# Performance work log

Measured on AMD Instinct MI355X. Metric: run time of the kernel, lower is better.

## Reference

```python
import jax, jax.numpy as jnp
import numpy as np

B = 2048          # batch (vmapped samples)
STEPS = 64        # hardcoded scan length in module
H = 64            # hidden_size
W = 128           # width_size
NZ = 32           # noise_size (control_size)
INZ = 32          # initial_noise_size
D = 8             # data_size


def lipswish(x):
    return 0.909 * jax.nn.silu(x)


def _mlp3(x, W0, b0, W1, b1, W2, b2, act, final_act):
    # eqx.nn.MLP with depth=2: in->width, width->width, width->out
    h = act(x @ W0.T + b0)
    h = act(h @ W1.T + b1)
    return final_act(h @ W2.T + b2)


def setup_inputs() -> dict:
    key = jax.random.key(0)
    ks = jax.random.split(key, 32)

    def lin(k, out_d, in_d):
        lim = 1.0 / np.sqrt(in_d)
        kw, kb = jax.random.split(k)
        Wm = jax.random.uniform(kw, (out_d, in_d), minval=-lim, maxval=lim, dtype=jnp.float32)
        bv = jax.random.uniform(kb, (out_d,), minval=-lim, maxval=lim, dtype=jnp.float32)
        return Wm, bv

    Wi0, bi0 = lin(ks[0], W, INZ)
    Wi1, bi1 = lin(ks[1], W, W)
    Wi2, bi2 = lin(ks[2], H, W)

    Wv0, bv0 = lin(ks[3], W, H + 1)
    Wv1, bv1 = lin(ks[4], W, W)
    Wv2, bv2 = lin(ks[5], H, W)
    scale_v = jax.random.uniform(ks[6], (H,), minval=0.9, maxval=1.1, dtype=jnp.float32)

    Wc0, bc0 = lin(ks[7], W, H + 1)
    Wc1, bc1 = lin(ks[8], W, W)
    Wc2, bc2 = lin(ks[9], H * NZ, W)
    scale_c = jax.random.uniform(ks[10], (H, NZ), minval=0.9, maxval=1.1, dtype=jnp.float32)

    Wr, br = lin(ks[11], D, H)

    ts = jnp.arange(STEPS + 1, dtype=jnp.float32)
    init_noise = jax.random.normal(ks[12], (B, INZ), dtype=jnp.float32)
    bm = jax.random.normal(ks[13], (B, STEPS, NZ), dtype=jnp.float32)

    return dict(ts=ts, init_noise=init_noise, bm=bm,
                Wi0=Wi0, bi0=bi0, Wi1=Wi1, bi1=bi1, Wi2=Wi2, bi2=bi2,
                scale_v=scale_v, Wv0=Wv0, bv0=bv0, Wv1=Wv1, bv1=bv1, Wv2=Wv2, bv2=bv2,
                scale_c=scale_c, Wc0=Wc0, bc0=bc0, Wc1=Wc1, bc1=bc1, Wc2=Wc2, bc2=bc2,
                Wr=Wr, br=br)


def reference(ts, init_noise, bm,
              Wi0, bi0, Wi1, bi1, Wi2, bi2,
              scale_v, Wv0, bv0, Wv1, bv1, Wv2, bv2,
              scale_c, Wc0, bc0, Wc1, bc1, Wc2, bc2,
              Wr, br):
    t0 = ts[0]
    dt = jnp.float32(1.0)  # dt0 hardcoded in module
    sqrt_dt = jnp.sqrt(dt)

    # initial MLP (relu hidden, identity final): noise -> y0 [B,H]
    y0 = _mlp3(init_noise, Wi0, bi0, Wi1, bi1, Wi2, bi2, jax.nn.relu, lambda x: x)

    bm_t = jnp.transpose(bm, (1, 0, 2))  # [STEPS, B, NZ]
    idx = jnp.arange(STEPS, dtype=jnp.float32)

    def step(y, xs):
        i, bm_i = xs
        t = t0 + i * dt
        tcol = jnp.broadcast_to(jnp.reshape(t, (1, 1)), (y.shape[0], 1))
        inp = jnp.concatenate([tcol, y], axis=1)  # [B, H+1]
        # drift vector field
        drift = scale_v * _mlp3(inp, Wv0, bv0, Wv1, bv1, Wv2, bv2, lipswish, jnp.tanh)
        # controlled vector field: [B, H, NZ]
        diff = scale_c * _mlp3(inp, Wc0, bc0, Wc1, bc1, Wc2, bc2, lipswish, jnp.tanh).reshape(-1, H, NZ)
        y1 = y + drift * dt + jnp.einsum('bhn,bn->bh', diff, bm_i * sqrt_dt)
        return y1, y1

    _, ys = jax.lax.scan(step, y0, (idx, bm_t), length=STEPS, unroll=8)  # ys [STEPS,B,H]
    out = jnp.einsum('tbh,dh->tbd', ys, Wr) + br  # readout per step
    return jnp.transpose(out, (1, 0, 2))  # [B, STEPS, D]
```

## Files before the change

kernel.cpp:

```cpp
#include <hip/hip_runtime.h>
#include <stdint.h>
#include <stddef.h>


typedef __attribute__((ext_vector_type(8))) short bf16x8;
typedef __attribute__((ext_vector_type(4))) float f32x4;
typedef __attribute__((ext_vector_type(4))) int   i32x4;

#define BB 16
#define NWG 256

#define WS_WI0 0
#define WS_WI1 8192
#define WS_WI2 40960
#define WS_WV0 57344
#define WS_WV1 73728
#define WS_WV2 106496
#define WS_WC0 122880
#define WS_WC1 139264
#define WS_WC2 172032
#define WS_TV0 696320
#define WS_TC0 696832
#define WS_XCHG 700416
#define WS_FLAG 2273280

#define LD_WV0 0
#define LD_WV1 16384
#define LD_WC0 49152
#define LD_WC1 65536
#define LD_YBF 98304
#define LD_H1V 100352
#define LD_H1C 104448
#define LD_H2V 108544
#define LD_H2C 112640
#define LD_Y   116736
#define LD_DB  121088
#define LD_BM  125440
#define LD_BSC 127552
#define LD_BEV 135744
#define LD_BEC 136256
#define LD_BV1 136768
#define LD_BC1 137280
#define LD_BV2 137792
#define LD_SV  138048
#define LD_WR  138304
#define LD_BR  140480
#define LD_WV2 140512
#define LD_DFL 148704
#define LDS_TOTAL 148712

__device__ __forceinline__ short f2bf(float f) {
  uint32_t u = __builtin_bit_cast(uint32_t, f);
  uint32_t r = (u + 0x7fffu + ((u >> 16) & 1u)) >> 16;
  return (short)r;
}
__device__ __forceinline__ float bf2f(short s) {
  uint32_t u = ((uint32_t)(uint16_t)s) << 16;
  return __builtin_bit_cast(float, u);
}
__device__ __forceinline__ uint32_t cvtpk(float lo, float hi) {
  uint32_t r;
  asm("v_cvt_pk_bf16_f32 %0, %1, %2" : "=v"(r) : "v"(lo), "v"(hi));
  return r;
}
__device__ __forceinline__ float tanh_fast(float x) {
  float e = __builtin_amdgcn_exp2f(x * 2.8853900817779268f);
  return __builtin_fmaf(-2.f, __builtin_amdgcn_rcpf(e + 1.f), 1.f);
}
__device__ __forceinline__ float lipswish(float x) {
  float s = __builtin_amdgcn_rcpf(1.f + __builtin_amdgcn_exp2f(-1.4426950408889634f * x));
  return 0.909f * x * s;
}
__device__ __forceinline__ float red16(float x) {
  int v;
  v = __builtin_amdgcn_update_dpp(0, __builtin_bit_cast(int, x), 0xB1, 0xF, 0xF, true);
  x += __builtin_bit_cast(float, v);
  v = __builtin_amdgcn_update_dpp(0, __builtin_bit_cast(int, x), 0x4E, 0xF, 0xF, true);
  x += __builtin_bit_cast(float, v);
  v = __builtin_amdgcn_update_dpp(0, __builtin_bit_cast(int, x), 0x141, 0xF, 0xF, true);
  x += __builtin_bit_cast(float, v);
  v = __builtin_amdgcn_update_dpp(0, __builtin_bit_cast(int, x), 0x140, 0xF, 0xF, true);
  x += __builtin_bit_cast(float, v);
  return x;
}
__device__ __forceinline__ void write_act(char* buf, int m, int k, short v) {
  int addr = ((k >> 5) << 10) + (m + ((k >> 3) & 3) * 16) * 16 + ((k & 7) << 1);
  *(short*)(buf + addr) = v;
}

template<int KF>
__device__ __forceinline__ f32x4 gemm_tile(const char* abase, const char* bbase, int lane) {
  f32x4 acc = {0.f, 0.f, 0.f, 0.f};
#pragma unroll
  for (int k = 0; k < KF; k++) {
    bf16x8 a = *(const bf16x8*)(abase + k * 1024 + lane * 16);
    bf16x8 b = *(const bf16x8*)(bbase + k * 1024 + lane * 16);
    acc = __builtin_amdgcn_mfma_f32_16x16x32_bf16(a, b, acc, 0, 0, 0);
  }
  return acc;
}

__global__ __launch_bounds__(256) void prep_kernel(
    const float* Wi0, const float* Wi1, const float* Wi2,
    const float* Wv0, const float* Wv1, const float* Wv2,
    const float* Wc0, const float* Wc1, const float* Wc2, char* ws) {
  int gid = blockIdx.x * 256 + threadIdx.x;
  if (gid < 4096) ((unsigned*)(ws + WS_FLAG))[gid] = 0;
  if (gid < 680 * 64) {
    int frag = gid >> 6, lane = gid & 63;
    const float* src; int start, KI, srcK, c0;
    if      (frag < 8)   { src = Wi0; start = 0;   KI = 1; srcK = 32;  c0 = 0; }
    else if (frag < 40)  { src = Wi1; start = 8;   KI = 4; srcK = 128; c0 = 0; }
    else if (frag < 56)  { src = Wi2; start = 40;  KI = 4; srcK = 128; c0 = 0; }
    else if (frag < 72)  { src = Wv0; start = 56;  KI = 2; srcK = 65;  c0 = 1; }
    else if (frag < 104) { src = Wv1; start = 72;  KI = 4; srcK = 128; c0 = 0; }
    else if (frag < 120) { src = Wv2; start = 104; KI = 4; srcK = 128; c0 = 0; }
    else if (frag < 136) { src = Wc0; start = 120; KI = 2; srcK = 65;  c0 = 1; }
    else if (frag < 168) { src = Wc1; start = 136; KI = 4; srcK = 128; c0 = 0; }
    else                 { src = Wc2; start = 168; KI = 4; srcK = 128; c0 = 0; }
    int rel = frag - start;
    int nt = rel / KI, ki = rel % KI;
    int n16 = lane & 15, quad = lane >> 4;
    const float* s = src + (nt * 16 + n16) * srcK + c0 + ki * 32 + quad * 8;
    bf16x8 v;
#pragma unroll
    for (int j = 0; j < 8; j++) v[j] = f2bf(s[j]);
    *(bf16x8*)(ws + (size_t)frag * 1024 + lane * 16) = v;
  } else {
    int i = gid - 680 * 64;
    if (i < 128)      ((float*)(ws + WS_TV0))[i] = Wv0[i * 65];
    else if (i < 256) ((float*)(ws + WS_TC0))[i - 128] = Wc0[(i - 128) * 65];
  }
}

__global__ __launch_bounds__(512, 2)
void sde_kernel(
    const float* ts, const float* init_noise, const float* bm,
    const float* bi0, const float* bi1, const float* bi2,
    const float* bv0, const float* bv1, const float* bv2, const float* scale_v,
    const float* bc0, const float* bc1, const float* bc2, const float* scale_c,
    const float* Wr, const float* br,
    char* ws, float* out) {
  extern __shared__ __align__(16) char lds[];
  const int tid  = threadIdx.x;
  const int lane = tid & 63;
  const int wv   = tid >> 6;
  const int nl   = lane & 15;
  const int quad = lane >> 4;
  const int bid  = blockIdx.x;
  const int ro   = (bid >> 3) & 1;
  const int pid  = ((bid >> 4) << 3) | (bid & 7);
  const int b0   = pid * BB;
  const int hbase = ro << 5;
  const char* wc2 = ws + WS_WC2 + (size_t)(ro * 64 + wv * 8) * 4096;
  char* xch = ws + WS_XCHG;
  unsigned* flags = (unsigned*)(ws + WS_FLAG);
  const int myflag = (pid << 1) | ro;
  const int paflag = (pid << 1) | (1 - ro);
  const float brv = (tid < 128) ? br[tid & 7] : 0.f;

  float tvq = 0.f, bbq = 0.f;
  if (tid >= 256) {
    int j = tid - 256;
    if (j < 128) { tvq = ((const float*)(ws + WS_TV0))[j];       bbq = bv0[j]; }
    else         { tvq = ((const float*)(ws + WS_TC0))[j - 128]; bbq = bc0[j - 128]; }
  }

  {
    const i32x4* s0 = (const i32x4*)(ws + WS_WV0);
    const i32x4* s1 = (const i32x4*)(ws + WS_WC0);
    i32x4* d0 = (i32x4*)(lds + LD_WV0);
    i32x4* d1 = (i32x4*)(lds + LD_WC0);
    for (int j = tid; j < 3072; j += 512) { d0[j] = s0[j]; d1[j] = s1[j]; }
  }
  {
    const i32x4* s2 = (const i32x4*)(ws + WS_WV2 + ro * 8192);
    ((i32x4*)(lds + LD_WV2))[tid] = s2[tid];
  }
  for (int j = tid; j < 2048; j += 512) {
    uint32_t u = (uint32_t)(uint16_t)f2bf(bc2[j]) |
                 ((uint32_t)(uint16_t)f2bf(scale_c[j]) << 16);
    ((uint32_t*)(lds + LD_BSC))[j] = u;
  }
  if (tid < 2) ((unsigned*)(lds + LD_DFL))[tid] = 0;
  if (tid < 128)      { ((float*)(lds + LD_BV1))[tid] = bv1[tid];
                        ((float*)(lds + LD_BC1))[tid] = bc1[tid]; }
  else if (tid < 192) { int k = tid - 128; ((float*)(lds + LD_BV2))[k] = bv2[k];
                        ((float*)(lds + LD_SV))[k] = scale_v[k]; }
  else if (tid < 200) { int k = tid - 192; ((float*)(lds + LD_BR))[k] = br[k]; }
  { int dd = tid >> 6, k = tid & 63;
    ((float*)(lds + LD_WR))[dd * 68 + k] = Wr[dd * 64 + k]; }
  { int m = tid >> 5, k = tid & 31;
    write_act(lds + LD_YBF, m, k, f2bf(init_noise[(b0 + m) * 32 + k])); }
  __syncthreads();

  { f32x4 acc = gemm_tile<1>(lds + LD_YBF, ws + WS_WI0 + wv * 1024, lane);
    int col = wv * 16 + nl; float bias = bi0[col];
#pragma unroll
    for (int r = 0; r < 4; r++)
      write_act(lds + LD_H1V, quad * 4 + r, col, f2bf(fmaxf(0.f, acc[r] + bias))); }
  __syncthreads();
  { f32x4 acc = gemm_tile<4>(lds + LD_H1V, ws + WS_WI1 + wv * 4096, lane);
    int col = wv * 16 + nl; float bias = bi1[col];
#pragma unroll
    for (int r = 0; r < 4; r++)
      write_act(lds + LD_H2V, quad * 4 + r, col, f2bf(fmaxf(0.f, acc[r] + bias))); }
  __syncthreads();
  if (wv < 4) {
    f32x4 acc = gemm_tile<4>(lds + LD_H2V, ws + WS_WI2 + wv * 4096, lane);
    int col = wv * 16 + nl; float bias = bi2[col];
#pragma unroll
    for (int r = 0; r < 4; r++)
      ((float*)(lds + LD_Y))[(quad * 4 + r) * 68 + col] = acc[r] + bias;
  }
  __syncthreads();

#define LOADT(N, OFF)                                                          \
  bf16x8 w##N##a = *(const bf16x8*)(wc2 + (OFF) +    0 + lane * 16);           \
  bf16x8 w##N##b = *(const bf16x8*)(wc2 + (OFF) + 1024 + lane * 16);           \
  bf16x8 w##N##c = *(const bf16x8*)(wc2 + (OFF) + 2048 + lane * 16);           \
  bf16x8 w##N##d = *(const bf16x8*)(wc2 + (OFF) + 3072 + lane * 16);
  LOADT(0, 0)     LOADT(1, 4096)  LOADT(2, 8192)  LOADT(3, 12288)
  LOADT(4, 16384) LOADT(5, 20480) LOADT(6, 24576) LOADT(7, 28672)
#undef LOADT

  const float ts0 = ts[0];
  for (int e = tid; e < 1024; e += 512) {
    int row = e >> 6, k = e & 63;
    write_act(lds + LD_YBF, row, k, f2bf(((float*)(lds + LD_Y))[row * 68 + k]));
  }
  ((float*)(lds + LD_BM))[(tid >> 5) * 33 + (tid & 31)] =
      bm[((size_t)(b0 + (tid >> 5)) * 64 + 0) * 32 + (tid & 31)];
  if (tid >= 256) {
    int j = tid - 256; float v = bbq + ts0 * tvq;
    if (j < 128) ((float*)(lds + LD_BEV))[j] = v;
    else         ((float*)(lds + LD_BEC))[j - 128] = v;
  }
  __syncthreads();

  for (int step = 0; step < 64; step++) {
    char* my_slot = xch + (size_t)(((myflag << 1) | (step & 1))) * 2048;
    const char* pa_slot = xch + (size_t)(((paflag << 1) | (step & 1))) * 2048;
    const unsigned want = (unsigned)(step + 1);
    {
      int col = wv * 16 + nl;
      f32x4 av = gemm_tile<2>(lds + LD_YBF, lds + LD_WV0 + wv * 2048, lane);
      f32x4 ac = gemm_tile<2>(lds + LD_YBF, lds + LD_WC0 + wv * 2048, lane);
      float bv = ((float*)(lds + LD_BEV))[col];
      float bc = ((float*)(lds + LD_BEC))[col];
      uint32_t p0 = cvtpk(lipswish(av[0] + bv), lipswish(av[1] + bv));
      uint32_t p1 = cvtpk(lipswish(av[2] + bv), lipswish(av[3] + bv));
      uint32_t q0 = cvtpk(lipswish(ac[0] + bc), lipswish(ac[1] + bc));
      uint32_t q1 = cvtpk(lipswish(ac[2] + bc), lipswish(ac[3] + bc));
      write_act(lds + LD_H1V, quad * 4 + 0, col, (short)p0);
      write_act(lds + LD_H1V, quad * 4 + 1, col, (short)(p0 >> 16));
      write_act(lds + LD_H1V, quad * 4 + 2, col, (short)p1);
      write_act(lds + LD_H1V, quad * 4 + 3, col, (short)(p1 >> 16));
      write_act(lds + LD_H1C, quad * 4 + 0, col, (short)q0);
      write_act(lds + LD_H1C, quad * 4 + 1, col, (short)(q0 >> 16));
      write_act(lds + LD_H1C, quad * 4 + 2, col, (short)q1);
      write_act(lds + LD_H1C, quad * 4 + 3, col, (short)(q1 >> 16));
    }
    __syncthreads();
    {
      int col = wv * 16 + nl;
      f32x4 av = gemm_tile<4>(lds + LD_H1V, lds + LD_WV1 + wv * 4096, lane);
      f32x4 ac = gemm_tile<4>(lds + LD_H1C, lds + LD_WC1 + wv * 4096, lane);
      float bv = ((float*)(lds + LD_BV1))[col];
      float bc = ((float*)(lds + LD_BC1))[col];
      uint32_t p0 = cvtpk(lipswish(av[0] + bv), lipswish(av[1] + bv));
      uint32_t p1 = cvtpk(lipswish(av[2] + bv), lipswish(av[3] + bv));
      uint32_t q0 = cvtpk(lipswish(ac[0] + bc), lipswish(ac[1] + bc));
      uint32_t q1 = cvtpk(lipswish(ac[2] + bc), lipswish(ac[3] + bc));
      write_act(lds + LD_H2V, quad * 4 + 0, col, (short)p0);
      write_act(lds + LD_H2V, quad * 4 + 1, col, (short)(p0 >> 16));
      write_act(lds + LD_H2V, quad * 4 + 2, col, (short)p1);
      write_act(lds + LD_H2V, quad * 4 + 3, col, (short)(p1 >> 16));
      write_act(lds + LD_H2C, quad * 4 + 0, col, (short)q0);
      write_act(lds + LD_H2C, quad * 4 + 1, col, (short)(q0 >> 16));
      write_act(lds + LD_H2C, quad * 4 + 2, col, (short)q1);
      write_act(lds + LD_H2C, quad * 4 + 3, col, (short)(q1 >> 16));
    }
    __syncthreads();
    float bm_next = 0.f;
    if (step + 1 < 64)
      bm_next = bm[((size_t)(b0 + (tid >> 5)) * 64 + (step + 1)) * 32 + (tid & 31)];
    if (wv < 2) {
      const char* vb = lds + LD_WV2 + wv * 4096;
      f32x4 acc = {0.f, 0.f, 0.f, 0.f};
      acc = __builtin_amdgcn_mfma_f32_16x16x32_bf16(
          *(const bf16x8*)(lds + LD_H2V +    0 + lane * 16),
          *(const bf16x8*)(vb +    0 + lane * 16), acc, 0, 0, 0);
      acc = __builtin_amdgcn_mfma_f32_16x16x32_bf16(
          *(const bf16x8*)(lds + LD_H2V + 1024 + lane * 16),
          *(const bf16x8*)(vb + 1024 + lane * 16), acc, 0, 0, 0);
      acc = __builtin_amdgcn_mfma_f32_16x16x32_bf16(
          *(const bf16x8*)(lds + LD_H2V + 2048 + lane * 16),
          *(const bf16x8*)(vb + 2048 + lane * 16), acc, 0, 0, 0);
      acc = __builtin_amdgcn_mfma_f32_16x16x32_bf16(
          *(const bf16x8*)(lds + LD_H2V + 3072 + lane * 16),
          *(const bf16x8*)(vb + 3072 + lane * 16), acc, 0, 0, 0);
      int col = (ro * 2 + wv) * 16 + nl;
      float bias = ((float*)(lds + LD_BV2))[col];
      float sv   = ((float*)(lds + LD_SV))[col];
#pragma unroll
      for (int r = 0; r < 4; r++)
        ((float*)(lds + LD_DB))[(quad * 4 + r) * 68 + col] = sv * tanh_fast(acc[r] + bias);
      asm volatile("s_waitcnt lgkmcnt(0)" ::: "memory");
      if (lane == 0) ((unsigned*)(lds + LD_DFL))[wv] = want;
    }
    {
      bf16x8 a0f = *(const bf16x8*)(lds + LD_H2C +    0 + lane * 16);
      bf16x8 a1f = *(const bf16x8*)(lds + LD_H2C + 1024 + lane * 16);
      bf16x8 a2f = *(const bf16x8*)(lds + LD_H2C + 2048 + lane * 16);
      bf16x8 a3f = *(const bf16x8*)(lds + LD_H2C + 3072 + lane * 16);
      const float* bmp = (const float*)(lds + LD_BM);
      float bmr00 = bmp[(quad * 4 + 0) * 33 + nl];
      float bmr01 = bmp[(quad * 4 + 1) * 33 + nl];
      float bmr02 = bmp[(quad * 4 + 2) * 33 + nl];
      float bmr03 = bmp[(quad * 4 + 3) * 33 + nl];
      float bmr10 = bmp[(quad * 4 + 0) * 33 + 16 + nl];
      float bmr11 = bmp[(quad * 4 + 1) * 33 + 16 + nl];
      float bmr12 = bmp[(quad * 4 + 2) * 33 + 16 + nl];
      float bmr13 = bmp[(quad * 4 + 3) * 33 + 16 + nl];
      const uint32_t* bscp = (const uint32_t*)(lds + LD_BSC) + (ro * 64 + wv * 8) * 16 + nl;
      float ps0, ps1, ps2, ps3;

#define DIFF_PAIR(P, E0, E1, E2, E3, O0, O1, O2, O3)                          \
      {                                                     \
        f32x4 acc = {0.f, 0.f, 0.f, 0.f};                                     \
        acc = __builtin_amdgcn_mfma_f32_16x16x32_bf16(a0f, E0, acc, 0, 0, 0); \
        acc = __builtin_amdgcn_mfma_f32_16x16x32_bf16(a1f, E1, acc, 0, 0, 0); \
        acc = __builtin_amdgcn_mfma_f32_16x16x32_bf16(a2f, E2, acc, 0, 0, 0); \
        acc = __builtin_amdgcn_mfma_f32_16x16x32_bf16(a3f, E3, acc, 0, 0, 0); \
        uint32_t bsc = bscp[(2*(P))*16];                                      \
        float bc2v = bf2f((short)(bsc & 0xffffu));                            \
        float scv  = bf2f((short)(bsc >> 16));                                \
        ps0 = tanh_fast(acc[0] + bc2v) * scv * bmr00;                         \
        ps1 = tanh_fast(acc[1] + bc2v) * scv * bmr01;                         \
        ps2 = tanh_fast(acc[2] + bc2v) * scv * bmr02;                         \
        ps3 = tanh_fast(acc[3] + bc2v) * scv * bmr03;                         \
      }                                                                       \
      float s##P;                                                             \
      {                                                    \
        f32x4 acc = {0.f, 0.f, 0.f, 0.f};                                     \
        acc = __builtin_amdgcn_mfma_f32_16x16x32_bf16(a0f, O0, acc, 0, 0, 0); \
        acc = __builtin_amdgcn_mfma_f32_16x16x32_bf16(a1f, O1, acc, 0, 0, 0); \
        acc = __builtin_amdgcn_mfma_f32_16x16x32_bf16(a2f, O2, acc, 0, 0, 0); \
        acc = __builtin_amdgcn_mfma_f32_16x16x32_bf16(a3f, O3, acc, 0, 0, 0); \
        uint32_t bsc = bscp[(2*(P)+1)*16];                                    \
        float bc2v = bf2f((short)(bsc & 0xffffu));                            \
        float scv  = bf2f((short)(bsc >> 16));                                \
        ps0 += tanh_fast(acc[0] + bc2v) * scv * bmr10;                        \
        ps1 += tanh_fast(acc[1] + bc2v) * scv * bmr11;                        \
        ps2 += tanh_fast(acc[2] + bc2v) * scv * bmr12;                        \
        ps3 += tanh_fast(acc[3] + bc2v) * scv * bmr13;                        \
        ps0 = red16(ps0); ps1 = red16(ps1); ps2 = red16(ps2); ps3 = red16(ps3);\
        s##P = (nl == 0) ? ps0 : (nl == 1) ? ps1 : (nl == 2) ? ps2 : ps3;     \
      }

      DIFF_PAIR(0, w0a, w0b, w0c, w0d, w1a, w1b, w1c, w1d)
      DIFF_PAIR(1, w2a, w2b, w2c, w2d, w3a, w3b, w3c, w3d)
      DIFF_PAIR(2, w4a, w4b, w4c, w4d, w5a, w5b, w5c, w5d)
      DIFF_PAIR(3, w6a, w6b, w6c, w6d, w7a, w7b, w7c, w7d)
#undef DIFF_PAIR

      {
        volatile unsigned* df = (volatile unsigned*)(lds + LD_DFL) + (wv >> 2);
        int g = 0;
        while (*df < want) { __builtin_amdgcn_s_sleep(0); if (++g > (1 << 20)) break; }
        __builtin_amdgcn_sched_barrier(0);
        if (nl < 4) {
          int row = quad * 4 + nl;
          int c0 = hbase + (wv << 2);
          f32x4 yv = *(const f32x4*)(lds + LD_Y  + (row * 68 + c0) * 4);
          f32x4 db = *(const f32x4*)(lds + LD_DB + (row * 68 + c0) * 4);
          f32x4 vn;
          vn[0] = (yv[0] + s0) + db[0];
          vn[1] = (yv[1] + s1) + db[1];
          vn[2] = (yv[2] + s2) + db[2];
          vn[3] = (yv[3] + s3) + db[3];
          *(f32x4*)(lds + LD_Y + (row * 68 + c0) * 4) = vn;
          uint32_t lo = cvtpk(vn[0], vn[1]);
          uint32_t hi = cvtpk(vn[2], vn[3]);
          uint64_t p64 = (uint64_t)lo | ((uint64_t)hi << 32);
          int inner = (row + (wv >> 1) * 16) * 16 + ((wv & 1) << 3);
          *(uint64_t*)(lds + LD_YBF + ro * 1024 + inner) = p64;
          __hip_atomic_store((unsigned long long*)(my_slot + inner),
                             (unsigned long long)p64,
                             __ATOMIC_RELAXED, __HIP_MEMORY_SCOPE_AGENT);
        }
        asm volatile("s_waitcnt vmcnt(0)" ::: "memory");
        if (lane == 0)
          __hip_atomic_store(flags + myflag * 16 + wv, want,
                             __ATOMIC_RELAXED, __HIP_MEMORY_SCOPE_AGENT);
      }
    }
    __syncthreads();
    float part = 0.f;
    if (tid < 128) {
      int row = tid >> 3, kq = tid & 7;
      const float* yr = (const float*)(lds + LD_Y) + row * 68 + hbase;
      const float* wr = (const float*)(lds + LD_WR) + kq * 68 + hbase;
#pragma unroll
      for (int j = 0; j < 8; j++) {
        f32x4 a = *(const f32x4*)(yr + j * 4);
        f32x4 w = *(const f32x4*)(wr + j * 4);
        part = fmaf(a[0], w[0], part); part = fmaf(a[1], w[1], part);
        part = fmaf(a[2], w[2], part); part = fmaf(a[3], w[3], part);
      }
      if ((tid >> 6) != ro)
        __hip_atomic_store((unsigned*)(my_slot + 1024) + (tid & 63),
                           __builtin_bit_cast(unsigned, part),
                           __ATOMIC_RELAXED, __HIP_MEMORY_SCOPE_AGENT);
      asm volatile("s_waitcnt vmcnt(0)" ::: "memory");
      if (lane == 0)
        __hip_atomic_store(flags + myflag * 16 + 8 + (tid >> 6), want,
                           __ATOMIC_RELAXED, __HIP_MEMORY_SCOPE_AGENT);
    } else if (tid >= 256 && step + 1 < 64) {
      int j = tid - 256; float v = bbq + (ts0 + (float)(step + 1)) * tvq;
      if (j < 128) ((float*)(lds + LD_BEV))[j] = v;
      else         ((float*)(lds + LD_BEC))[j - 128] = v;
    }
    if (step + 1 < 64)
      ((float*)(lds + LD_BM))[(tid >> 5) * 33 + (tid & 31)] = bm_next;
    if (tid < 128) {
      const unsigned long long* sf = (const unsigned long long*)(flags + paflag * 16);
      int g = 0;
      for (;;) {
        unsigned long long f0 = __hip_atomic_load(sf + 0, __ATOMIC_RELAXED, __HIP_MEMORY_SCOPE_AGENT);
        unsigned long long f1 = __hip_atomic_load(sf + 1, __ATOMIC_RELAXED, __HIP_MEMORY_SCOPE_AGENT);
        unsigned long long f2 = __hip_atomic_load(sf + 2, __ATOMIC_RELAXED, __HIP_MEMORY_SCOPE_AGENT);
        unsigned long long f3 = __hip_atomic_load(sf + 3, __ATOMIC_RELAXED, __HIP_MEMORY_SCOPE_AGENT);
        if ((unsigned)f0 >= want && (unsigned)(f0 >> 32) >= want &&
            (unsigned)f1 >= want && (unsigned)(f1 >> 32) >= want &&
            (unsigned)f2 >= want && (unsigned)(f2 >> 32) >= want &&
            (unsigned)f3 >= want && (unsigned)(f3 >> 32) >= want) break;
        __builtin_amdgcn_s_sleep(1);
        if (++g > (1 << 20)) break;
      }
      unsigned long long v = __hip_atomic_load((const unsigned long long*)pa_slot + tid,
                                               __ATOMIC_RELAXED, __HIP_MEMORY_SCOPE_AGENT);
      *(unsigned long long*)(lds + LD_YBF + (1 - ro) * 1024 + tid * 8) = v;
      if ((tid >> 6) == ro) {
        int g2 = 0;
        for (;;) {
          unsigned long long fp = __hip_atomic_load(sf + 4, __ATOMIC_RELAXED, __HIP_MEMORY_SCOPE_AGENT);
          if ((unsigned)fp >= want && (unsigned)(fp >> 32) >= want) break;
          __builtin_amdgcn_s_sleep(1);
          if (++g2 > (1 << 20)) break;
        }
        float pp = __builtin_bit_cast(float, __hip_atomic_load(
            (const unsigned*)(pa_slot + 1024) + (tid & 63),
            __ATOMIC_RELAXED, __HIP_MEMORY_SCOPE_AGENT));
        int row = tid >> 3, dd = tid & 7;
        out[(size_t)(b0 + row) * 512 + step * 8 + dd] = part + pp + brv;
      }
    }
    __syncthreads();
  }
}

extern "C" void kernel_launch(void* const* d_in, const int* in_sizes, int n_in,
                              void* d_out, int out_size, void* d_ws, size_t ws_size,
                              hipStream_t stream) {
  (void)in_sizes; (void)n_in; (void)out_size; (void)ws_size;
  const float* ts         = (const float*)d_in[0];
  const float* init_noise = (const float*)d_in[1];
  const float* bm         = (const float*)d_in[2];
  const float* Wi0 = (const float*)d_in[3];
  const float* bi0 = (const float*)d_in[4];
  const float* Wi1 = (const float*)d_in[5];
  const float* bi1 = (const float*)d_in[6];
  const float* Wi2 = (const float*)d_in[7];
  const float* bi2 = (const float*)d_in[8];
  const float* scale_v = (const float*)d_in[9];
  const float* Wv0 = (const float*)d_in[10];
  const float* bv0 = (const float*)d_in[11];
  const float* Wv1 = (const float*)d_in[12];
  const float* bv1 = (const float*)d_in[13];
  const float* Wv2 = (const float*)d_in[14];
  const float* bv2 = (const float*)d_in[15];
  const float* scale_c = (const float*)d_in[16];
  const float* Wc0 = (const float*)d_in[17];
  const float* bc0 = (const float*)d_in[18];
  const float* Wc1 = (const float*)d_in[19];
  const float* bc1 = (const float*)d_in[20];
  const float* Wc2 = (const float*)d_in[21];
  const float* bc2 = (const float*)d_in[22];
  const float* Wr  = (const float*)d_in[23];
  const float* br  = (const float*)d_in[24];
  char*  ws  = (char*)d_ws;
  float* out = (float*)d_out;

  hipFuncSetAttribute((const void*)sde_kernel,
                      hipFuncAttributeMaxDynamicSharedMemorySize, LDS_TOTAL);

  prep_kernel<<<171, 256, 0, stream>>>(Wi0, Wi1, Wi2, Wv0, Wv1, Wv2, Wc0, Wc1, Wc2, ws);
  sde_kernel<<<NWG, 512, LDS_TOTAL, stream>>>(
      ts, init_noise, bm, bi0, bi1, bi2, bv0, bv1, bv2, scale_v,
      bc0, bc1, bc2, scale_c, Wr, br, ws, out);
}
```

Measured before the change: 461.0 us.

## Defer readout by one step and consolidate state update into one wave group

Moves the per-step readout dot product and its cross-workgroup partial-sum exchange off the critical path by computing the previous step's readout after the next step's hidden layers. Diffusion partial sums now go to a new LDS buffer. A dedicated group of threads then does the state update, exchanges it with the partner workgroup and polls a single 64-bit flag instead of eight. This replaces the LDS flag spin between waves. The aim is to shorten the serialized inter-workgroup synchronization chain each step. The cost is an extra epilogue for the last step and a different flag layout that depends on careful ordering.

```diff
diff --git a/kernel.cpp b/kernel.cpp
--- a/kernel.cpp
+++ b/kernel.cpp
@@ -9,6 +9,7 @@
 
 #define BB 16
 #define NWG 256
+#define SPIN_GUARD (1 << 18)
 
 #define WS_WI0 0
 #define WS_WI1 8192
@@ -46,8 +47,8 @@
 #define LD_WR  138304
 #define LD_BR  140480
 #define LD_WV2 140512
-#define LD_DFL 148704
-#define LDS_TOTAL 148712
+#define LD_DS  148704
+#define LDS_TOTAL 151008
 
 __device__ __forceinline__ short f2bf(float f) {
   uint32_t u = __builtin_bit_cast(uint32_t, f);
@@ -157,13 +158,13 @@
   unsigned* flags = (unsigned*)(ws + WS_FLAG);
   const int myflag = (pid << 1) | ro;
   const int paflag = (pid << 1) | (1 - ro);
-  const float brv = (tid < 128) ? br[tid & 7] : 0.f;
-
-  float tvq = 0.f, bbq = 0.f;
-  if (tid >= 256) {
+  const float brv = (tid >= 128 && tid < 256) ? br[tid & 7] : 0.f;
+
+  float tvqv = 0.f, bbqv = 0.f, tvqc = 0.f, bbqc = 0.f;
+  if (tid >= 256 && tid < 384) {
     int j = tid - 256;
-    if (j < 128) { tvq = ((const float*)(ws + WS_TV0))[j];       bbq = bv0[j]; }
-    else         { tvq = ((const float*)(ws + WS_TC0))[j - 128]; bbq = bc0[j - 128]; }
+    tvqv = ((const float*)(ws + WS_TV0))[j];  bbqv = bv0[j];
+    tvqc = ((const float*)(ws + WS_TC0))[j];  bbqc = bc0[j];
   }
 
   {
@@ -182,7 +183,6 @@
                  ((uint32_t)(uint16_t)f2bf(scale_c[j]) << 16);
     ((uint32_t*)(lds + LD_BSC))[j] = u;
   }
-  if (tid < 2) ((unsigned*)(lds + LD_DFL))[tid] = 0;
   if (tid < 128)      { ((float*)(lds + LD_BV1))[tid] = bv1[tid];
                         ((float*)(lds + LD_BC1))[tid] = bc1[tid]; }
   else if (tid < 192) { int k = tid - 128; ((float*)(lds + LD_BV2))[k] = bv2[k];
@@ -231,16 +231,14 @@
   }
   ((float*)(lds + LD_BM))[(tid >> 5) * 33 + (tid & 31)] =
       bm[((size_t)(b0 + (tid >> 5)) * 64 + 0) * 32 + (tid & 31)];
-  if (tid >= 256) {
-    int j = tid - 256; float v = bbq + ts0 * tvq;
-    if (j < 128) ((float*)(lds + LD_BEV))[j] = v;
-    else         ((float*)(lds + LD_BEC))[j - 128] = v;
+  if (tid >= 256 && tid < 384) {
+    int j = tid - 256;
+    ((float*)(lds + LD_BEV))[j] = bbqv + ts0 * tvqv;
+    ((float*)(lds + LD_BEC))[j] = bbqc + ts0 * tvqc;
   }
   __syncthreads();
 
   for (int step = 0; step < 64; step++) {
-    char* my_slot = xch + (size_t)(((myflag << 1) | (step & 1))) * 2048;
-    const char* pa_slot = xch + (size_t)(((paflag << 1) | (step & 1))) * 2048;
     const unsigned want = (unsigned)(step + 1);
     {
       int col = wv * 16 + nl;
@@ -282,6 +280,43 @@
       write_act(lds + LD_H2C, quad * 4 + 3, col, (short)(q1 >> 16));
     }
     __syncthreads();
+    if (step > 0 && tid >= 128 && tid < 256) {
+      int j = tid - 128;
+      int row = j >> 3, kq = j & 7;
+      const float* yr = (const float*)(lds + LD_Y) + row * 68 + hbase;
+      const float* wr = (const float*)(lds + LD_WR) + kq * 68 + hbase;
+      float part = 0.f;
+#pragma unroll
+      for (int i = 0; i < 8; i++) {
+        f32x4 a = *(const f32x4*)(yr + i * 4);
+        f32x4 w = *(const f32x4*)(wr + i * 4);
+        part = fmaf(a[0], w[0], part); part = fmaf(a[1], w[1], part);
+        part = fmaf(a[2], w[2], part); part = fmaf(a[3], w[3], part);
+      }
+      int pparity = (step - 1) & 1;
+      char* mslot = xch + (size_t)((myflag << 1) | pparity) * 2048;
+      const char* pslot = xch + (size_t)((paflag << 1) | pparity) * 2048;
+      if ((j >> 6) == (1 - ro)) {
+        __hip_atomic_store((unsigned*)(mslot + 1024) + (j & 63),
+                           __builtin_bit_cast(unsigned, part),
+                           __ATOMIC_RELAXED, __HIP_MEMORY_SCOPE_AGENT);
+        asm volatile("s_waitcnt vmcnt(0)" ::: "memory");
+        if ((j & 63) == 0)
+          __hip_atomic_store(flags + myflag * 4 + 2, (unsigned)step,
+                             __ATOMIC_RELAXED, __HIP_MEMORY_SCOPE_AGENT);
+      } else {
+        int g = 0;
+        while (__hip_atomic_load(flags + paflag * 4 + 2, __ATOMIC_RELAXED,
+                                 __HIP_MEMORY_SCOPE_AGENT) < (unsigned)step) {
+          __builtin_amdgcn_s_sleep(1);
+          if (++g > SPIN_GUARD) break;
+        }
+        float pp = __builtin_bit_cast(float, __hip_atomic_load(
+            (const unsigned*)(pslot + 1024) + (j & 63),
+            __ATOMIC_RELAXED, __HIP_MEMORY_SCOPE_AGENT));
+        out[(size_t)(b0 + row) * 512 + (step - 1) * 8 + kq] = part + pp + brv;
+      }
+    }
     float bm_next = 0.f;
     if (step + 1 < 64)
       bm_next = bm[((size_t)(b0 + (tid >> 5)) * 64 + (step + 1)) * 32 + (tid & 31)];
@@ -306,8 +341,6 @@
 #pragma unroll
       for (int r = 0; r < 4; r++)
         ((float*)(lds + LD_DB))[(quad * 4 + r) * 68 + col] = sv * tanh_fast(acc[r] + bias);
-      asm volatile("s_waitcnt lgkmcnt(0)" ::: "memory");
-      if (lane == 0) ((unsigned*)(lds + LD_DFL))[wv] = want;
     }
     {
       bf16x8 a0f = *(const bf16x8*)(lds + LD_H2C +    0 + lane * 16);
@@ -341,7 +374,6 @@
         ps2 = tanh_fast(acc[2] + bc2v) * scv * bmr02;                         \
         ps3 = tanh_fast(acc[3] + bc2v) * scv * bmr03;                         \
       }                                                                       \
-      float s##P;                                                             \
       {                                                    \
         f32x4 acc = {0.f, 0.f, 0.f, 0.f};                                     \
         acc = __builtin_amdgcn_mfma_f32_16x16x32_bf16(a0f, O0, acc, 0, 0, 0); \
@@ -356,7 +388,11 @@
         ps2 += tanh_fast(acc[2] + bc2v) * scv * bmr12;                        \
         ps3 += tanh_fast(acc[3] + bc2v) * scv * bmr13;                        \
         ps0 = red16(ps0); ps1 = red16(ps1); ps2 = red16(ps2); ps3 = red16(ps3);\
-        s##P = (nl == 0) ? ps0 : (nl == 1) ? ps1 : (nl == 2) ? ps2 : ps3;     \
+        if (nl < 4) {                                                         \
+          int row = quad * 4 + nl;                                            \
+          float s = (nl == 0) ? ps0 : (nl == 1) ? ps1 : (nl == 2) ? ps2 : ps3;\
+          ((float*)(lds + LD_DS))[row * 36 + (wv << 2) + (P)] = s;            \
+        }                                                                     \
       }
 
       DIFF_PAIR(0, w0a, w0b, w0c, w0d, w1a, w1b, w1c, w1d)
@@ -364,100 +400,92 @@
       DIFF_PAIR(2, w4a, w4b, w4c, w4d, w5a, w5b, w5c, w5d)
       DIFF_PAIR(3, w6a, w6b, w6c, w6d, w7a, w7b, w7c, w7d)
 #undef DIFF_PAIR
-
-      {
-        volatile unsigned* df = (volatile unsigned*)(lds + LD_DFL) + (wv >> 2);
-        int g = 0;
-        while (*df < want) { __builtin_amdgcn_s_sleep(0); if (++g > (1 << 20)) break; }
-        __builtin_amdgcn_sched_barrier(0);
-        if (nl < 4) {
-          int row = quad * 4 + nl;
-          int c0 = hbase + (wv << 2);
-          f32x4 yv = *(const f32x4*)(lds + LD_Y  + (row * 68 + c0) * 4);
-          f32x4 db = *(const f32x4*)(lds + LD_DB + (row * 68 + c0) * 4);
-          f32x4 vn;
-          vn[0] = (yv[0] + s0) + db[0];
-          vn[1] = (yv[1] + s1) + db[1];
-          vn[2] = (yv[2] + s2) + db[2];
-          vn[3] = (yv[3] + s3) + db[3];
-          *(f32x4*)(lds + LD_Y + (row * 68 + c0) * 4) = vn;
-          uint32_t lo = cvtpk(vn[0], vn[1]);
-          uint32_t hi = cvtpk(vn[2], vn[3]);
-          uint64_t p64 = (uint64_t)lo | ((uint64_t)hi << 32);
-          int inner = (row + (wv >> 1) * 16) * 16 + ((wv & 1) << 3);
-          *(uint64_t*)(lds + LD_YBF + ro * 1024 + inner) = p64;
-          __hip_atomic_store((unsigned long long*)(my_slot + inner),
-                             (unsigned long long)p64,
-                             __ATOMIC_RELAXED, __HIP_MEMORY_SCOPE_AGENT);
-        }
-        asm volatile("s_waitcnt vmcnt(0)" ::: "memory");
-        if (lane == 0)
-          __hip_atomic_store(flags + myflag * 16 + wv, want,
-                             __ATOMIC_RELAXED, __HIP_MEMORY_SCOPE_AGENT);
-      }
     }
     __syncthreads();
-    float part = 0.f;
-    if (tid < 128) {
-      int row = tid >> 3, kq = tid & 7;
-      const float* yr = (const float*)(lds + LD_Y) + row * 68 + hbase;
-      const float* wr = (const float*)(lds + LD_WR) + kq * 68 + hbase;
-#pragma unroll
-      for (int j = 0; j < 8; j++) {
-        f32x4 a = *(const f32x4*)(yr + j * 4);
-        f32x4 w = *(const f32x4*)(wr + j * 4);
-        part = fmaf(a[0], w[0], part); part = fmaf(a[1], w[1], part);
-        part = fmaf(a[2], w[2], part); part = fmaf(a[3], w[3], part);
-      }
-      if ((tid >> 6) != ro)
-        __hip_atomic_store((unsigned*)(my_slot + 1024) + (tid & 63),
-                           __builtin_bit_cast(unsigned, part),
-                           __ATOMIC_RELAXED, __HIP_MEMORY_SCOPE_AGENT);
+    if (step + 1 < 64)
+      ((float*)(lds + LD_BM))[(tid >> 5) * 33 + (tid & 31)] = bm_next;
+    char* my_slot = xch + (size_t)(((myflag << 1) | (step & 1))) * 2048;
+    const char* pa_slot = xch + (size_t)(((paflag << 1) | (step & 1))) * 2048;
+    if (tid >= 384) {
+      int j = tid - 384;
+      int row = j >> 3, kq = j & 7;
+      int c0 = hbase + kq * 4;
+      f32x4 yv = *(const f32x4*)(lds + LD_Y  + (row * 68 + c0) * 4);
+      f32x4 sv4 = *(const f32x4*)(lds + LD_DS + (row * 36 + kq * 4) * 4);
+      f32x4 db = *(const f32x4*)(lds + LD_DB + (row * 68 + c0) * 4);
+      f32x4 vn;
+      vn[0] = (yv[0] + sv4[0]) + db[0];
+      vn[1] = (yv[1] + sv4[1]) + db[1];
+      vn[2] = (yv[2] + sv4[2]) + db[2];
+      vn[3] = (yv[3] + sv4[3]) + db[3];
+      *(f32x4*)(lds + LD_Y + (row * 68 + c0) * 4) = vn;
+      uint32_t lo = cvtpk(vn[0], vn[1]);
+      uint32_t hi = cvtpk(vn[2], vn[3]);
+      uint64_t p64 = (uint64_t)lo | ((uint64_t)hi << 32);
+      int inner = (row + (kq >> 1) * 16) * 16 + ((kq & 1) << 3);
+      *(uint64_t*)(lds + LD_YBF + ro * 1024 + inner) = p64;
+      __hip_atomic_store((unsigned long long*)(my_slot + inner),
+                         (unsigned long long)p64,
+                         __ATOMIC_RELAXED, __HIP_MEMORY_SCOPE_AGENT);
       asm volatile("s_waitcnt vmcnt(0)" ::: "memory");
       if (lane == 0)
-        __hip_atomic_store(flags + myflag * 16 + 8 + (tid >> 6), want,
+        __hip_atomic_store(flags + myflag * 4 + ((tid >> 6) & 1), want,
                            __ATOMIC_RELAXED, __HIP_MEMORY_SCOPE_AGENT);
-    } else if (tid >= 256 && step + 1 < 64) {
-      int j = tid - 256; float v = bbq + (ts0 + (float)(step + 1)) * tvq;
-      if (j < 128) ((float*)(lds + LD_BEV))[j] = v;
-      else         ((float*)(lds + LD_BEC))[j - 128] = v;
-    }
-    if (step + 1 < 64)
-      ((float*)(lds + LD_BM))[(tid >> 5) * 33 + (tid & 31)] = bm_next;
-    if (tid < 128) {
-      const unsigned long long* sf = (const unsigned long long*)(flags + paflag * 16);
+      const unsigned long long* pfl = (const unsigned long long*)(flags + paflag * 4);
       int g = 0;
       for (;;) {
-        unsigned long long f0 = __hip_atomic_load(sf + 0, __ATOMIC_RELAXED, __HIP_MEMORY_SCOPE_AGENT);
-        unsigned long long f1 = __hip_atomic_load(sf + 1, __ATOMIC_RELAXED, __HIP_MEMORY_SCOPE_AGENT);
-        unsigned long long f2 = __hip_atomic_load(sf + 2, __ATOMIC_RELAXED, __HIP_MEMORY_SCOPE_AGENT);
-        unsigned long long f3 = __hip_atomic_load(sf + 3, __ATOMIC_RELAXED, __HIP_MEMORY_SCOPE_AGENT);
-        if ((unsigned)f0 >= want && (unsigned)(f0 >> 32) >= want &&
-            (unsigned)f1 >= want && (unsigned)(f1 >> 32) >= want &&
-            (unsigned)f2 >= want && (unsigned)(f2 >> 32) >= want &&
-            (unsigned)f3 >= want && (unsigned)(f3 >> 32) >= want) break;
+        unsigned long long fv = __hip_atomic_load(pfl, __ATOMIC_RELAXED,
+                                                  __HIP_MEMORY_SCOPE_AGENT);
+        if ((unsigned)fv >= want && (unsigned)(fv >> 32) >= want) break;
         __builtin_amdgcn_s_sleep(1);
-        if (++g > (1 << 20)) break;
+        if (++g > SPIN_GUARD) break;
       }
-      unsigned long long v = __hip_atomic_load((const unsigned long long*)pa_slot + tid,
+      unsigned long long v = __hip_atomic_load((const unsigned long long*)pa_slot + j,
                                                __ATOMIC_RELAXED, __HIP_MEMORY_SCOPE_AGENT);
-      *(unsigned long long*)(lds + LD_YBF + (1 - ro) * 1024 + tid * 8) = v;
-      if ((tid >> 6) == ro) {
-        int g2 = 0;
-        for (;;) {
-          unsigned long long fp = __hip_atomic_load(sf + 4, __ATOMIC_RELAXED, __HIP_MEMORY_SCOPE_AGENT);
-          if ((unsigned)fp >= want && (unsigned)(fp >> 32) >= want) break;
-          __builtin_amdgcn_s_sleep(1);
-          if (++g2 > (1 << 20)) break;
-        }
-        float pp = __builtin_bit_cast(float, __hip_atomic_load(
-            (const unsigned*)(pa_slot + 1024) + (tid & 63),
-            __ATOMIC_RELAXED, __HIP_MEMORY_SCOPE_AGENT));
-        int row = tid >> 3, dd = tid & 7;
-        out[(size_t)(b0 + row) * 512 + step * 8 + dd] = part + pp + brv;
+      *(unsigned long long*)(lds + LD_YBF + (1 - ro) * 1024 + j * 8) = v;
+    } else if (tid >= 256 && step + 1 < 64) {
+      int j = tid - 256; float t = ts0 + (float)(step + 1);
+      ((float*)(lds + LD_BEV))[j] = bbqv + t * tvqv;
+      ((float*)(lds + LD_BEC))[j] = bbqc + t * tvqc;
+    }
+    __syncthreads();
+  }
+
+  if (tid >= 128 && tid < 256) {
+    int j = tid - 128;
+    int row = j >> 3, kq = j & 7;
+    const float* yr = (const float*)(lds + LD_Y) + row * 68 + hbase;
+    const float* wr = (const float*)(lds + LD_WR) + kq * 68 + hbase;
+    float part = 0.f;
+#pragma unroll
+    for (int i = 0; i < 8; i++) {
+      f32x4 a = *(const f32x4*)(yr + i * 4);
+      f32x4 w = *(const f32x4*)(wr + i * 4);
+      part = fmaf(a[0], w[0], part); part = fmaf(a[1], w[1], part);
+      part = fmaf(a[2], w[2], part); part = fmaf(a[3], w[3], part);
+    }
+    char* mslot = xch + (size_t)((myflag << 1) | 1) * 2048;
+    const char* pslot = xch + (size_t)((paflag << 1) | 1) * 2048;
+    if ((j >> 6) == (1 - ro)) {
+      __hip_atomic_store((unsigned*)(mslot + 1024) + (j & 63),
+                         __builtin_bit_cast(unsigned, part),
+                         __ATOMIC_RELAXED, __HIP_MEMORY_SCOPE_AGENT);
+      asm volatile("s_waitcnt vmcnt(0)" ::: "memory");
+      if ((j & 63) == 0)
+        __hip_atomic_store(flags + myflag * 4 + 2, 64u,
+                           __ATOMIC_RELAXED, __HIP_MEMORY_SCOPE_AGENT);
+    } else {
+      int g = 0;
+      while (__hip_atomic_load(flags + paflag * 4 + 2, __ATOMIC_RELAXED,
+                               __HIP_MEMORY_SCOPE_AGENT) < 64u) {
+        __builtin_amdgcn_s_sleep(1);
+        if (++g > SPIN_GUARD) break;
       }
-    }
-    __syncthreads();
+      float pp = __builtin_bit_cast(float, __hip_atomic_load(
+          (const unsigned*)(pslot + 1024) + (j & 63),
+          __ATOMIC_RELAXED, __HIP_MEMORY_SCOPE_AGENT));
+      out[(size_t)(b0 + row) * 512 + 63 * 8 + kq] = part + pp + brv;
+    }
   }
 }
 
```

New measurement: 469.4 us. Within noise of the previous version (+1.8%).
